# Performance work log

Measured on AMD Instinct MI355X. Metric: run time of the kernel, lower is better.

The kernel has to match this reference:

```python
import jax, jax.numpy as jnp
import numpy as np

FDS = [80, 160, 400, 600]
N, E, G, IN = 20000, 320000, 128, 3072
EPS = 1e-5  # BatchNorm1d default eps


def setup_inputs():
    key = jax.random.key(0)
    ks = iter(jax.random.split(key, 64))
    inp = {}
    inp["x"] = jax.random.normal(next(ks), (N, IN), jnp.float32)
    inp["edge_index"] = jax.random.randint(next(ks), (2, E), 0, N)
    inp["batch"] = jnp.sort(jax.random.randint(next(ks), (N,), 0, G))
    for i, fd in enumerate(FDS):
        din = IN if i == 0 else FDS[i - 1]
        def u(shape, fan):
            s = 1.0 / np.sqrt(fan)
            return jax.random.uniform(next(ks), shape, jnp.float32, -s, s)
        inp[f"wa{i}"] = u((din, 4 * fd), din)      # Linear(din, 4*fd)
        inp[f"ba{i}"] = u((4 * fd,), din)
        inp[f"wb{i}"] = u((4 * fd, fd), 4 * fd)    # Linear(4*fd, fd)
        inp[f"bb{i}"] = u((fd,), 4 * fd)
        inp[f"gw{i}"] = u((fd, fd), fd)            # GCNConv weight
        inp[f"gb{i}"] = jnp.zeros((fd,), jnp.float32)  # GCNConv bias
        inp[f"gamma{i}"] = jnp.ones((fd,), jnp.float32)
        inp[f"beta{i}"] = jnp.zeros((fd,), jnp.float32)
        inp[f"mean{i}"] = jax.random.normal(next(ks), (fd,), jnp.float32) * 0.1
        inp[f"var{i}"] = jax.random.uniform(next(ks), (fd,), jnp.float32, 0.5, 1.5)
    return inp


def _gcn_edges(edge_index, n):
    # GCNConv default: add self-loops, symmetric D^-1/2 (A+I) D^-1/2 normalization
    loops = jnp.arange(n)
    src = jnp.concatenate([edge_index[0], loops])
    dst = jnp.concatenate([edge_index[1], loops])
    deg = jax.ops.segment_sum(jnp.ones(src.shape, jnp.float32), dst, num_segments=n)
    dinv = jnp.where(deg > 0, jax.lax.rsqrt(deg), 0.0)
    return src, dst, dinv[src] * dinv[dst]


def _forward(x, edge_index, batch, params):
    src, dst, norm = _gcn_edges(edge_index, N)
    for (wa, ba, wb, bb, gw, gb, gamma, beta, mean, var) in params:
        h = jax.nn.relu(x @ wa + ba)   # dropout = identity in eval mode
        h = jax.nn.relu(h @ wb + bb)
        h = h @ gw                     # GCN linear transform
        # gather -> normalize -> scatter-add message passing, then bias
        h = jax.ops.segment_sum(h[src] * norm[:, None], dst, num_segments=N) + gb
        # BatchNorm1d (eval: running stats)
        h = (h - mean) * jax.lax.rsqrt(var + EPS) * gamma + beta
        x = jax.nn.relu(h)             # residual branch is dead: dims never match
    return jax.ops.segment_max(x, batch, num_segments=G)  # global_max_pool


def reference(x, edge_index, batch,
              wa0, ba0, wb0, bb0, gw0, gb0, gamma0, beta0, mean0, var0,
              wa1, ba1, wb1, bb1, gw1, gb1, gamma1, beta1, mean1, var1,
              wa2, ba2, wb2, bb2, gw2, gb2, gamma2, beta2, mean2, var2,
              wa3, ba3, wb3, bb3, gw3, gb3, gamma3, beta3, mean3, var3):
    params = [
        (wa0, ba0, wb0, bb0, gw0, gb0, gamma0, beta0, mean0, var0),
        (wa1, ba1, wb1, bb1, gw1, gb1, gamma1, beta1, mean1, var1),
        (wa2, ba2, wb2, bb2, gw2, gb2, gamma2, beta2, mean2, var2),
        (wa3, ba3, wb3, bb3, gw3, gb3, gamma3, beta3, mean3, var3),
    ]
    return _forward(x, edge_index, batch, params)
```

## Files before the change

### kernel.cpp

```cpp
#include <hip/hip_runtime.h>
#include <cstdint>
#include <cstddef>
#include <cmath>


#define EPS_BN 1e-5f

typedef unsigned short u16;
typedef short short8 __attribute__((ext_vector_type(8)));
typedef u16 u16x8 __attribute__((ext_vector_type(8)));
typedef u16 u16x4 __attribute__((ext_vector_type(4)));
typedef float fx4 __attribute__((ext_vector_type(4)));

__device__ __forceinline__ u16 bf16_rn(float f) {
  unsigned u = __float_as_uint(f);
  return (u16)((u + 0x7FFFu + ((u >> 16) & 1u)) >> 16);
}
__device__ __forceinline__ float bf16_f(u16 h) {
  return __uint_as_float(((unsigned)h) << 16);
}

__device__ __forceinline__ void gload16(const void* g, void* l) {
  __builtin_amdgcn_global_load_lds(
      (const __attribute__((address_space(1))) void*)g,
      (__attribute__((address_space(3))) void*)l, 16, 0, 0);
}

__device__ __forceinline__ void map_tile(int b, int tm, int tn, int T,
                                         int& mt, int& nt) {
  const int x = b & 7;
  const int s = b >> 3;
  const int cap = ((tm - x + 7) >> 3) * tn;
  if (s < cap) {
    const int q = s / tn;
    mt = x + (q << 3);
    nt = s - q * tn;
    return;
  }
  int r = s - cap;
  for (int xp = 0; xp < x; ++xp) {
    const int nbp = (T - xp + 7) >> 3;
    const int capp = ((tm - xp + 7) >> 3) * tn;
    if (nbp > capp) r += nbp - capp;
  }
  for (int xq = 0; xq < 8; ++xq) {
    const int nbq = (T - xq + 7) >> 3;
    const int capq = ((tm - xq + 7) >> 3) * tn;
    const int def = capq - nbq;
    if (def > 0) {
      if (r < def) {
        const int sq = nbq + r;
        const int q = sq / tn;
        mt = xq + (q << 3);
        nt = sq - q * tn;
        return;
      }
      r -= def;
    }
  }
  mt = 0; nt = 0;
}

template <int OUTMODE, bool SPLITA>
__global__ __launch_bounds__(256, 2) void gemm_mfma(
    const u16* __restrict__ Ahi, const u16* __restrict__ Alo,
    const float* __restrict__ Af,
    const u16* __restrict__ Bhi, const u16* __restrict__ Blo,
    const float* __restrict__ bias,
    float* __restrict__ Cf, u16* __restrict__ Chi, u16* __restrict__ Clo,
    int M, int N, int K, int lda, int ldb, int ldc, int tm, int tn) {
  __shared__ __align__(16) u16 As[2][128 * 32];
  __shared__ __align__(16) u16 Bs[2][128 * 32];

  int mt, nt;
  map_tile(blockIdx.x, tm, tn, tm * tn, mt, nt);
  const int m0 = mt * 128;
  const int n0 = nt * 128;

  const int tid = threadIdx.x;
  const int lane = tid & 63;
  const int wid = tid >> 6;
  const int wm = (wid >> 1) * 64;
  const int wn = (wid & 1) * 64;
  const int quad = lane >> 4;
  const int l15 = lane & 15;

  const int srow = tid >> 2;
  const int sg = ((tid & 3) ^ srow ^ (srow >> 2)) & 3;
  int ar0 = m0 + srow;      if (ar0 >= M) ar0 = M - 1;
  int ar1 = m0 + srow + 64; if (ar1 >= M) ar1 = M - 1;
  int br0 = n0 + srow;      if (br0 >= N) br0 = N - 1;
  int br1 = n0 + srow + 64; if (br1 >= N) br1 = N - 1;
  const size_t aof0 = (size_t)ar0 * lda + (sg << 3);
  const size_t aof1 = (size_t)ar1 * lda + (sg << 3);
  const size_t bof0 = (size_t)br0 * ldb + (sg << 3);
  const size_t bof1 = (size_t)br1 * ldb + (sg << 3);
  const int l0 = wid << 9;
  const int l1 = 2048 + (wid << 9);
  const int wls = srow * 32 + ((tid & 3) << 3);

  fx4 zf = {0.f, 0.f, 0.f, 0.f};
  fx4 acc[4][4];
#pragma unroll
  for (int a = 0; a < 4; ++a)
#pragma unroll
    for (int b = 0; b < 4; ++b) acc[a][b] = zf;

  const int nk = (K + 31) >> 5;
  for (int ki = 0; ki < nk; ++ki) {
    const int k0 = ki << 5;
    u16x8 va_h[2], va_l[2];
    if (SPLITA) {
#pragma unroll
      for (int it = 0; it < 2; ++it) {
        const float* pp = Af + (it ? aof1 : aof0) + k0;
        const fx4 f0 = *(const fx4*)pp;
        const fx4 f1 = *(const fx4*)(pp + 4);
        u16x8 h, l;
#pragma unroll
        for (int j = 0; j < 4; ++j) {
          const u16 hb = bf16_rn(f0[j]);
          h[j] = hb;
          l[j] = bf16_rn(f0[j] - bf16_f(hb));
        }
#pragma unroll
        for (int j = 0; j < 4; ++j) {
          const u16 hb = bf16_rn(f1[j]);
          h[4 + j] = hb;
          l[4 + j] = bf16_rn(f1[j] - bf16_f(hb));
        }
        va_h[it] = h;
        va_l[it] = l;
      }
    }

    if (ki) __syncthreads();

    if (SPLITA) {
      gload16(Bhi + bof0 + k0, &Bs[0][l0]);
      gload16(Bhi + bof1 + k0, &Bs[0][l1]);
      gload16(Blo + bof0 + k0, &Bs[1][l0]);
      gload16(Blo + bof1 + k0, &Bs[1][l1]);
      *(u16x8*)&As[0][wls] = va_h[0];
      *(u16x8*)&As[0][wls + 2048] = va_h[1];
      *(u16x8*)&As[1][wls] = va_l[0];
      *(u16x8*)&As[1][wls + 2048] = va_l[1];
    } else {
      gload16(Ahi + aof0 + k0, &As[0][l0]);
      gload16(Ahi + aof1 + k0, &As[0][l1]);
      gload16(Alo + aof0 + k0, &As[1][l0]);
      gload16(Alo + aof1 + k0, &As[1][l1]);
      gload16(Bhi + bof0 + k0, &Bs[0][l0]);
      gload16(Bhi + bof1 + k0, &Bs[0][l1]);
      gload16(Blo + bof0 + k0, &Bs[1][l0]);
      gload16(Blo + bof1 + k0, &Bs[1][l1]);
    }
    __syncthreads();

    short8 ah[4], al[4], bh[4], bl[4];
#pragma unroll
    for (int t = 0; t < 4; ++t) {
      const int rA = wm + t * 16 + l15;
      const int oa = rA * 32 + (((quad ^ rA ^ (rA >> 2)) & 3) << 3);
      ah[t] = *(const short8*)&As[0][oa];
      al[t] = *(const short8*)&As[1][oa];
      const int rB = wn + t * 16 + l15;
      const int ob = rB * 32 + (((quad ^ rB ^ (rB >> 2)) & 3) << 3);
      bh[t] = *(const short8*)&Bs[0][ob];
      bl[t] = *(const short8*)&Bs[1][ob];
    }
#pragma unroll
    for (int a = 0; a < 4; ++a)
#pragma unroll
      for (int b = 0; b < 4; ++b) {
        acc[a][b] = __builtin_amdgcn_mfma_f32_16x16x32_bf16(ah[a], bh[b], acc[a][b], 0, 0, 0);
        acc[a][b] = __builtin_amdgcn_mfma_f32_16x16x32_bf16(ah[a], bl[b], acc[a][b], 0, 0, 0);
        acc[a][b] = __builtin_amdgcn_mfma_f32_16x16x32_bf16(al[a], bh[b], acc[a][b], 0, 0, 0);
      }
  }

#pragma unroll
  for (int a = 0; a < 4; ++a)
#pragma unroll
    for (int b = 0; b < 4; ++b) {
      const int gn = n0 + wn + b * 16 + l15;
      if (gn >= ldc) continue;
      const bool live = gn < N;
      const float bv = (OUTMODE == 1 && live) ? bias[gn] : 0.f;
#pragma unroll
      for (int r = 0; r < 4; ++r) {
        const int gm = m0 + wm + a * 16 + quad * 4 + r;
        if (gm >= M) continue;
        float v = live ? acc[a][b][r] : 0.f;
        if (OUTMODE == 1) {
          v = live ? fmaxf(v + bv, 0.f) : 0.f;
          const u16 hb = bf16_rn(v);
          Chi[(size_t)gm * ldc + gn] = hb;
          Clo[(size_t)gm * ldc + gn] = bf16_rn(v - bf16_f(hb));
        } else {
          Cf[(size_t)gm * ldc + gn] = v;
        }
      }
    }
}

struct TSJob { const float* W; u16* Th; u16* Tl; int K; int Kp; int N; int tiles_k; int base; };
struct TSJobs { TSJob j[12]; };

__global__ __launch_bounds__(256) void transpose_split_all(TSJobs jobs, int njobs) {
  const int b = blockIdx.x;
  int ji = 0;
  while (ji + 1 < njobs && jobs.j[ji + 1].base <= b) ++ji;
  const TSJob J = jobs.j[ji];
  const int t = b - J.base;
  const int k0 = (t % J.tiles_k) * 32;
  const int n0 = (t / J.tiles_k) * 32;
  __shared__ float tile[32][33];
  const int tx = threadIdx.x & 31, ty = threadIdx.x >> 5;
#pragma unroll
  for (int i = 0; i < 32; i += 8) {
    const int k = k0 + ty + i, n = n0 + tx;
    tile[ty + i][tx] = (k < J.K && n < J.N) ? J.W[(size_t)k * J.N + n] : 0.f;
  }
  __syncthreads();
#pragma unroll
  for (int i = 0; i < 32; i += 8) {
    const int n = n0 + ty + i, k = k0 + tx;
    if (n < J.N && k < J.Kp) {
      const float f = tile[tx][ty + i];
      const u16 hb = bf16_rn(f);
      J.Th[(size_t)n * J.Kp + k] = hb;
      J.Tl[(size_t)n * J.Kp + k] = bf16_rn(f - bf16_f(hb));
    }
  }
}

__global__ void count_deg(const int* __restrict__ dst, int E, int* __restrict__ cnt) {
  int e = blockIdx.x * blockDim.x + threadIdx.x;
  if (e < E) atomicAdd(&cnt[dst[e]], 1);
}

__global__ void compute_dinv(const int* __restrict__ cnt, float* __restrict__ dinv, int N) {
  int i = blockIdx.x * blockDim.x + threadIdx.x;
  if (i < N) dinv[i] = rsqrtf((float)(cnt[i] + 1));
}

__global__ void scan_block(const int* __restrict__ cnt, int* __restrict__ partial,
                           int* __restrict__ blocksum, int N) {
  __shared__ int s[256];
  const int t = threadIdx.x;
  const int i = blockIdx.x * 256 + t;
  int v = (i < N) ? cnt[i] : 0;
  s[t] = v;
  __syncthreads();
  for (int off = 1; off < 256; off <<= 1) {
    int u = (t >= off) ? s[t - off] : 0;
    __syncthreads();
    s[t] += u;
    __syncthreads();
  }
  if (i < N) partial[i] = s[t];
  if (t == 255) blocksum[blockIdx.x] = s[255];
}

__global__ void scan_sums(int* __restrict__ blocksum, int NB) {
  __shared__ int s[256];
  const int t = threadIdx.x;
  int v = (t < NB) ? blocksum[t] : 0;
  s[t] = v;
  __syncthreads();
  for (int off = 1; off < 256; off <<= 1) {
    int u = (t >= off) ? s[t - off] : 0;
    __syncthreads();
    s[t] += u;
    __syncthreads();
  }
  if (t < NB) blocksum[t] = s[t] - v;
}

__global__ void finalize_rowptr(const int* __restrict__ partial, const int* __restrict__ blockoff,
                                int* __restrict__ rowptr, int N) {
  int i = blockIdx.x * 256 + threadIdx.x;
  if (i < N) rowptr[i + 1] = partial[i] + blockoff[blockIdx.x];
  if (i == 0) rowptr[0] = 0;
}

__global__ void fill_csr(const int* __restrict__ src, const int* __restrict__ dst, int E,
                         const int* __restrict__ rowptr, int* __restrict__ cursor,
                         int* __restrict__ colidx) {
  int e = blockIdx.x * blockDim.x + threadIdx.x;
  if (e < E) {
    int d = dst[e];
    int p = atomicAdd(&cursor[d], 1);
    colidx[rowptr[d] + p] = src[e];
  }
}

__global__ void mp_bn_relu(
    const float* __restrict__ H, const int* __restrict__ rowptr,
    const int* __restrict__ colidx, const float* __restrict__ dinv,
    const float* __restrict__ gb, const float* __restrict__ gamma,
    const float* __restrict__ beta, const float* __restrict__ mean,
    const float* __restrict__ var,
    u16* __restrict__ Xh, u16* __restrict__ Xl, int N, int F, int Fp) {
  const int nch = Fp >> 2;
  const int idx = blockIdx.x * blockDim.x + threadIdx.x;
  if (idx >= N * nch) return;
  const int i = idx / nch;
  const int c = idx - i * nch;
  const size_t rowi = (size_t)i * Fp + (c << 2);
  if ((c << 2) >= F) {
    const u16x4 z = {0, 0, 0, 0};
    *(u16x4*)(Xh + rowi) = z;
    *(u16x4*)(Xl + rowi) = z;
    return;
  }
  const float di = dinv[i];
  fx4 acc = (di * di) * *(const fx4*)(H + rowi);
  const int e0 = rowptr[i], e1 = rowptr[i + 1];
  int e = e0;
  for (; e + 4 <= e1; e += 4) {
    const int s0 = colidx[e + 0], s1 = colidx[e + 1];
    const int s2 = colidx[e + 2], s3 = colidx[e + 3];
    const float w0 = di * dinv[s0], w1 = di * dinv[s1];
    const float w2 = di * dinv[s2], w3 = di * dinv[s3];
    const fx4 v0 = *(const fx4*)(H + (size_t)s0 * Fp + (c << 2));
    const fx4 v1 = *(const fx4*)(H + (size_t)s1 * Fp + (c << 2));
    const fx4 v2 = *(const fx4*)(H + (size_t)s2 * Fp + (c << 2));
    const fx4 v3 = *(const fx4*)(H + (size_t)s3 * Fp + (c << 2));
    acc += w0 * v0;
    acc += w1 * v1;
    acc += w2 * v2;
    acc += w3 * v3;
  }
  for (; e < e1; ++e) {
    const int s = colidx[e];
    acc += (di * dinv[s]) * *(const fx4*)(H + (size_t)s * Fp + (c << 2));
  }
  u16x4 oh, ol;
#pragma unroll
  for (int j = 0; j < 4; ++j) {
    const int col = (c << 2) + j;
    float v = (acc[j] + gb[col] - mean[col]) * rsqrtf(var[col] + EPS_BN) * gamma[col] + beta[col];
    v = fmaxf(v, 0.f);
    const u16 hb = bf16_rn(v);
    oh[j] = hb;
    ol[j] = bf16_rn(v - bf16_f(hb));
  }
  *(u16x4*)(Xh + rowi) = oh;
  *(u16x4*)(Xl + rowi) = ol;
}

__global__ void pool_seg(const u16* __restrict__ Xh, const u16* __restrict__ Xl,
                         const int* __restrict__ batch, float* __restrict__ out,
                         int N, int F, int ldx) {
  const int g = blockIdx.x;
  int lo = 0, hi = N;
  while (lo < hi) { int m = (lo + hi) >> 1; if (batch[m] < g) lo = m + 1; else hi = m; }
  const int s0 = lo;
  hi = N;
  while (lo < hi) { int m = (lo + hi) >> 1; if (batch[m] <= g) lo = m + 1; else hi = m; }
  const int s1 = lo;
  const int c = threadIdx.x;
  if (c * 4 >= F) return;
  fx4 mx = {-INFINITY, -INFINITY, -INFINITY, -INFINITY};
  for (int i = s0; i < s1; ++i) {
    const size_t off = (size_t)i * ldx + (c << 2);
    const u16x4 h = *(const u16x4*)(Xh + off);
    const u16x4 l = *(const u16x4*)(Xl + off);
#pragma unroll
    for (int j = 0; j < 4; ++j) mx[j] = fmaxf(mx[j], bf16_f(h[j]) + bf16_f(l[j]));
  }
  *(fx4*)(out + (size_t)g * F + (c << 2)) = mx;
}

extern "C" void kernel_launch(void* const* d_in, const int* in_sizes, int n_in,
                              void* d_out, int out_size, void* d_ws, size_t ws_size,
                              hipStream_t stream) {
  const float* x = (const float*)d_in[0];
  const int* edges = (const int*)d_in[1];
  const int* batch = (const int*)d_in[2];
  const int E = in_sizes[1] / 2;
  const int Nn = in_sizes[2];

  static const int FDS[4]  = {80, 160, 400, 600};
  static const int FDP[4]  = {96, 160, 416, 608};
  static const int DINS[4] = {3072, 80, 160, 400};
  static const int DINP[4] = {3072, 96, 160, 416};
  const float *wa[4], *ba[4], *wb[4], *bb[4], *gw[4], *gb[4], *gamma[4], *beta[4], *mean[4], *var[4];
  for (int i = 0; i < 4; ++i) {
    const int b = 3 + 10 * i;
    wa[i] = (const float*)d_in[b + 0];
    ba[i] = (const float*)d_in[b + 1];
    wb[i] = (const float*)d_in[b + 2];
    bb[i] = (const float*)d_in[b + 3];
    gw[i] = (const float*)d_in[b + 4];
    gb[i] = (const float*)d_in[b + 5];
    gamma[i] = (const float*)d_in[b + 6];
    beta[i] = (const float*)d_in[b + 7];
    mean[i] = (const float*)d_in[b + 8];
    var[i] = (const float*)d_in[b + 9];
  }

  char* p = (char*)d_ws;
  auto alloc = [&](size_t bytes) {
    char* r = p;
    p += (bytes + 255) & ~(size_t)255;
    return r;
  };
  u16* actA_h = (u16*)alloc((size_t)Nn * 2400 * 2);
  u16* actA_l = (u16*)alloc((size_t)Nn * 2400 * 2);
  u16* actB_h = (u16*)alloc((size_t)Nn * 608 * 2);
  u16* actB_l = (u16*)alloc((size_t)Nn * 608 * 2);
  float* H3 = (float*)actA_h;

  u16 *waT_h[4], *waT_l[4], *wbT_h[4], *wbT_l[4], *gwT_h[4], *gwT_l[4];
  for (int i = 0; i < 4; ++i) {
    const size_t s1 = (size_t)4 * FDS[i] * DINP[i];
    const size_t s2 = (size_t)FDS[i] * 4 * FDS[i];
    const size_t s3 = (size_t)FDS[i] * FDP[i];
    waT_h[i] = (u16*)alloc(s1 * 2);
    waT_l[i] = (u16*)alloc(s1 * 2);
    wbT_h[i] = (u16*)alloc(s2 * 2);
    wbT_l[i] = (u16*)alloc(s2 * 2);
    gwT_h[i] = (u16*)alloc(s3 * 2);
    gwT_l[i] = (u16*)alloc(s3 * 2);
  }

  int* cnt = (int*)alloc((size_t)Nn * sizeof(int));
  int* cursor = (int*)alloc((size_t)Nn * sizeof(int));
  int* partial = (int*)alloc((size_t)Nn * sizeof(int));
  int* blocksum = (int*)alloc(256 * sizeof(int));
  int* rowptr = (int*)alloc((size_t)(Nn + 1) * sizeof(int));
  int* colidx = (int*)alloc((size_t)E * sizeof(int));
  float* dinv = (float*)alloc((size_t)Nn * sizeof(float));

  const int* srcIdx = edges;
  const int* dstIdx = edges + E;

  {
    TSJobs jobs;
    int base = 0, ji = 0;
    auto addjob = [&](const float* W, int K, int Kp, int Ncols, u16* Th, u16* Tl) {
      const int tk = Kp / 32, tn = (Ncols + 31) / 32;
      jobs.j[ji++] = TSJob{W, Th, Tl, K, Kp, Ncols, tk, base};
      base += tk * tn;
    };
    for (int i = 0; i < 4; ++i) {
      addjob(wa[i], DINS[i], DINP[i], 4 * FDS[i], waT_h[i], waT_l[i]);
      addjob(wb[i], 4 * FDS[i], 4 * FDS[i], FDS[i], wbT_h[i], wbT_l[i]);
      addjob(gw[i], FDS[i], FDP[i], FDS[i], gwT_h[i], gwT_l[i]);
    }
    transpose_split_all<<<base, 256, 0, stream>>>(jobs, 12);
  }

  hipMemsetAsync(cnt, 0, (size_t)Nn * sizeof(int), stream);
  hipMemsetAsync(cursor, 0, (size_t)Nn * sizeof(int), stream);

  const int EB = (E + 255) / 256;
  const int NB = (Nn + 255) / 256;
  count_deg<<<EB, 256, 0, stream>>>(dstIdx, E, cnt);
  compute_dinv<<<NB, 256, 0, stream>>>(cnt, dinv, Nn);
  scan_block<<<NB, 256, 0, stream>>>(cnt, partial, blocksum, Nn);
  scan_sums<<<1, 256, 0, stream>>>(blocksum, NB);
  finalize_rowptr<<<NB, 256, 0, stream>>>(partial, blocksum, rowptr, Nn);
  fill_csr<<<EB, 256, 0, stream>>>(srcIdx, dstIdx, E, rowptr, cursor, colidx);

  const int tm = (Nn + 127) / 128;
  for (int i = 0; i < 4; ++i) {
    const int fd = FDS[i], fdp = FDP[i];
    const int hid = 4 * fd;
    const int din = DINS[i], dinp = DINP[i];

    {
      const int tn = (hid + 127) / 128;
      if (i == 0) {
        gemm_mfma<1, true><<<tm * tn, 256, 0, stream>>>(
            nullptr, nullptr, x, waT_h[0], waT_l[0], ba[0],
            nullptr, actA_h, actA_l, Nn, hid, din, din, dinp, hid, tm, tn);
      } else {
        gemm_mfma<1, false><<<tm * tn, 256, 0, stream>>>(
            actB_h, actB_l, nullptr, waT_h[i], waT_l[i], ba[i],
            nullptr, actA_h, actA_l, Nn, hid, din, dinp, dinp, hid, tm, tn);
      }
    }
    {
      const int tn = (fd + 127) / 128;
      gemm_mfma<1, false><<<tm * tn, 256, 0, stream>>>(
          actA_h, actA_l, nullptr, wbT_h[i], wbT_l[i], bb[i],
          nullptr, actB_h, actB_l, Nn, fd, hid, hid, hid, fdp, tm, tn);
    }
    {
      const int tn = (fd + 127) / 128;
      gemm_mfma<0, false><<<tm * tn, 256, 0, stream>>>(
          actB_h, actB_l, nullptr, gwT_h[i], gwT_l[i], nullptr,
          H3, nullptr, nullptr, Nn, fd, fd, fdp, fdp, fdp, tm, tn);
    }
    {
      const int items = Nn * (fdp >> 2);
      mp_bn_relu<<<(items + 255) / 256, 256, 0, stream>>>(
          H3, rowptr, colidx, dinv, gb[i], gamma[i], beta[i], mean[i], var[i],
          actB_h, actB_l, Nn, fd, fdp);
    }
  }

  pool_seg<<<out_size / 600, 192, 0, stream>>>(actB_h, actB_l, batch, (float*)d_out,
                                               Nn, 600, 608);
}
```

Before: 1.692 ms.

## Add double-buffered, phase-interleaved MFMA GEMM for bf16-split activation inputs

Splits the GEMM into a dedicated fp32-input split kernel and a new double-buffered kernel for pre-split bf16 inputs. The new kernel prefetches tiles two steps ahead into a second LDS buffer and waits with explicit vmcnt. Within each K step it issues the next tile's global-to-LDS loads spread across waves, interleaved between MFMA sub-blocks. It also raises MFMA priority with s_setprio, aiming to hide load latency behind compute. LDS use doubles to 64KB per block, which may hurt occupancy at 2 blocks per CU, and the many barriers add sync overhead.

Result: slower. 1.850 ms (+9.3%).

```diff
diff --git a/kernel.cpp b/kernel.cpp
--- a/kernel.cpp
+++ b/kernel.cpp
@@ -25,6 +25,8 @@
       (const __attribute__((address_space(1))) void*)g,
       (__attribute__((address_space(3))) void*)l, 16, 0, 0);
 }
+
+#define MEMFENCE() asm volatile("" ::: "memory")
 
 __device__ __forceinline__ void map_tile(int b, int tm, int tn, int T,
                                          int& mt, int& nt) {
@@ -61,13 +63,165 @@
   mt = 0; nt = 0;
 }
 
-template <int OUTMODE, bool SPLITA>
-__global__ __launch_bounds__(256, 2) void gemm_mfma(
+template <int OUTMODE>
+__global__ __launch_bounds__(256, 2) void gemm_ph(
     const u16* __restrict__ Ahi, const u16* __restrict__ Alo,
+    const u16* __restrict__ Bhi, const u16* __restrict__ Blo,
+    const float* __restrict__ bias,
+    float* __restrict__ Cf, u16* __restrict__ Chi, u16* __restrict__ Clo,
+    int M, int N, int K, int lda, int ldb, int ldc, int tm, int tn) {
+  __shared__ __align__(16) u16 As[2][2][128 * 32];
+  __shared__ __align__(16) u16 Bs[2][2][128 * 32];
+
+  int mt, nt;
+  map_tile(blockIdx.x, tm, tn, tm * tn, mt, nt);
+  const int m0 = mt * 128;
+  const int n0 = nt * 128;
+
+  const int tid = threadIdx.x;
+  const int lane = tid & 63;
+  const int wid = tid >> 6;
+  const int wm = (wid >> 1) * 64;
+  const int wn = (wid & 1) * 64;
+  const int quad = lane >> 4;
+  const int l15 = lane & 15;
+
+  const int srow = tid >> 2;
+  const int sg = ((tid & 3) ^ srow ^ (srow >> 2)) & 3;
+  int ar0 = m0 + srow;      if (ar0 >= M) ar0 = M - 1;
+  int ar1 = m0 + srow + 64; if (ar1 >= M) ar1 = M - 1;
+  int br0 = n0 + srow;      if (br0 >= N) br0 = N - 1;
+  int br1 = n0 + srow + 64; if (br1 >= N) br1 = N - 1;
+  const size_t aof0 = (size_t)ar0 * lda + (sg << 3);
+  const size_t aof1 = (size_t)ar1 * lda + (sg << 3);
+  const size_t bof0 = (size_t)br0 * ldb + (sg << 3);
+  const size_t bof1 = (size_t)br1 * ldb + (sg << 3);
+  const int l0 = wid << 9;
+  const int l1 = 2048 + (wid << 9);
+
+  fx4 zf = {0.f, 0.f, 0.f, 0.f};
+  fx4 acc[4][4];
+#pragma unroll
+  for (int a = 0; a < 4; ++a)
+#pragma unroll
+    for (int b = 0; b < 4; ++b) acc[a][b] = zf;
+
+  const int nk = (K + 31) >> 5;
+
+  auto stageA = [&](int kt, int bufi) {
+    const size_t kk = (size_t)kt << 5;
+    gload16(Ahi + aof0 + kk, &As[bufi][0][l0]);
+    gload16(Ahi + aof1 + kk, &As[bufi][0][l1]);
+    gload16(Alo + aof0 + kk, &As[bufi][1][l0]);
+    gload16(Alo + aof1 + kk, &As[bufi][1][l1]);
+  };
+  auto stageB = [&](int kt, int bufi) {
+    const size_t kk = (size_t)kt << 5;
+    gload16(Bhi + bof0 + kk, &Bs[bufi][0][l0]);
+    gload16(Bhi + bof1 + kk, &Bs[bufi][0][l1]);
+    gload16(Blo + bof0 + kk, &Bs[bufi][1][l0]);
+    gload16(Blo + bof1 + kk, &Bs[bufi][1][l1]);
+  };
+
+  stageA(0, 0); stageB(0, 0);
+  if (nk > 1) { stageA(1, 1); stageB(1, 1); }
+  if (nk > 1) asm volatile("s_waitcnt vmcnt(8)" ::: "memory");
+  else        asm volatile("s_waitcnt vmcnt(0)" ::: "memory");
+  __builtin_amdgcn_s_barrier();
+  MEMFENCE();
+
+  for (int ki = 0; ki < nk; ++ki) {
+    const int cur = ki & 1;
+    const bool st = (ki + 2) < nk;
+
+    short8 bh[4], bl[4], ah, al;
+#pragma unroll
+    for (int t = 0; t < 4; ++t) {
+      const int rB = wn + t * 16 + l15;
+      const int ob = rB * 32 + (((quad ^ rB ^ (rB >> 2)) & 3) << 3);
+      bh[t] = *(const short8*)&Bs[cur][0][ob];
+      bl[t] = *(const short8*)&Bs[cur][1][ob];
+    }
+    {
+      const int rA = wm + l15;
+      const int oa = rA * 32 + (((quad ^ rA ^ (rA >> 2)) & 3) << 3);
+      ah = *(const short8*)&As[cur][0][oa];
+      al = *(const short8*)&As[cur][1][oa];
+    }
+    __builtin_amdgcn_s_setprio(1);
+#pragma unroll
+    for (int b = 0; b < 4; ++b) {
+      acc[0][b] = __builtin_amdgcn_mfma_f32_16x16x32_bf16(ah, bh[b], acc[0][b], 0, 0, 0);
+      acc[0][b] = __builtin_amdgcn_mfma_f32_16x16x32_bf16(ah, bl[b], acc[0][b], 0, 0, 0);
+      acc[0][b] = __builtin_amdgcn_mfma_f32_16x16x32_bf16(al, bh[b], acc[0][b], 0, 0, 0);
+    }
+    __builtin_amdgcn_s_setprio(0);
+    MEMFENCE();
+    __builtin_amdgcn_s_barrier();
+    MEMFENCE();
+
+#pragma unroll
+    for (int t = 1; t < 4; ++t) {
+      const int rA = wm + t * 16 + l15;
+      const int oa = rA * 32 + (((quad ^ rA ^ (rA >> 2)) & 3) << 3);
+      ah = *(const short8*)&As[cur][0][oa];
+      al = *(const short8*)&As[cur][1][oa];
+      if (t == 1 && st) {
+        stageB(ki + 2, cur);
+        if (wid == 0) stageA(ki + 2, cur);
+      }
+      if (t == 2 && st && wid == 1) stageA(ki + 2, cur);
+      if (t == 3 && st && wid == 2) stageA(ki + 2, cur);
+      __builtin_amdgcn_s_setprio(1);
+#pragma unroll
+      for (int b = 0; b < 4; ++b) {
+        acc[t][b] = __builtin_amdgcn_mfma_f32_16x16x32_bf16(ah, bh[b], acc[t][b], 0, 0, 0);
+        acc[t][b] = __builtin_amdgcn_mfma_f32_16x16x32_bf16(ah, bl[b], acc[t][b], 0, 0, 0);
+        acc[t][b] = __builtin_amdgcn_mfma_f32_16x16x32_bf16(al, bh[b], acc[t][b], 0, 0, 0);
+      }
+      __builtin_amdgcn_s_setprio(0);
+      MEMFENCE();
+      __builtin_amdgcn_s_barrier();
+      MEMFENCE();
+    }
+    if (st && wid == 3) stageA(ki + 2, cur);
+    if (st)                asm volatile("s_waitcnt vmcnt(8)" ::: "memory");
+    else if (ki + 1 < nk)  asm volatile("s_waitcnt vmcnt(0)" ::: "memory");
+    MEMFENCE();
+    __builtin_amdgcn_s_barrier();
+    MEMFENCE();
+  }
+
+#pragma unroll
+  for (int a = 0; a < 4; ++a)
+#pragma unroll
+    for (int b = 0; b < 4; ++b) {
+      const int gn = n0 + wn + b * 16 + l15;
+      if (gn >= ldc) continue;
+      const bool live = gn < N;
+      const float bv = (OUTMODE == 1 && live) ? bias[gn] : 0.f;
+#pragma unroll
+      for (int r = 0; r < 4; ++r) {
+        const int gm = m0 + wm + a * 16 + quad * 4 + r;
+        if (gm >= M) continue;
+        float v = live ? acc[a][b][r] : 0.f;
+        if (OUTMODE == 1) {
+          v = live ? fmaxf(v + bv, 0.f) : 0.f;
+          const u16 hb = bf16_rn(v);
+          Chi[(size_t)gm * ldc + gn] = hb;
+          Clo[(size_t)gm * ldc + gn] = bf16_rn(v - bf16_f(hb));
+        } else {
+          Cf[(size_t)gm * ldc + gn] = v;
+        }
+      }
+    }
+}
+
+__global__ __launch_bounds__(256, 2) void gemm_splita(
     const float* __restrict__ Af,
     const u16* __restrict__ Bhi, const u16* __restrict__ Blo,
     const float* __restrict__ bias,
-    float* __restrict__ Cf, u16* __restrict__ Chi, u16* __restrict__ Clo,
+    u16* __restrict__ Chi, u16* __restrict__ Clo,
     int M, int N, int K, int lda, int ldb, int ldc, int tm, int tn) {
   __shared__ __align__(16) u16 As[2][128 * 32];
   __shared__ __align__(16) u16 Bs[2][128 * 32];
@@ -110,51 +264,38 @@
   for (int ki = 0; ki < nk; ++ki) {
     const int k0 = ki << 5;
     u16x8 va_h[2], va_l[2];
-    if (SPLITA) {
-#pragma unroll
-      for (int it = 0; it < 2; ++it) {
-        const float* pp = Af + (it ? aof1 : aof0) + k0;
-        const fx4 f0 = *(const fx4*)pp;
-        const fx4 f1 = *(const fx4*)(pp + 4);
-        u16x8 h, l;
-#pragma unroll
-        for (int j = 0; j < 4; ++j) {
-          const u16 hb = bf16_rn(f0[j]);
-          h[j] = hb;
-          l[j] = bf16_rn(f0[j] - bf16_f(hb));
-        }
-#pragma unroll
-        for (int j = 0; j < 4; ++j) {
-          const u16 hb = bf16_rn(f1[j]);
-          h[4 + j] = hb;
-          l[4 + j] = bf16_rn(f1[j] - bf16_f(hb));
-        }
-        va_h[it] = h;
-        va_l[it] = l;
-      }
+#pragma unroll
+    for (int it = 0; it < 2; ++it) {
+      const float* pp = Af + (it ? aof1 : aof0) + k0;
+      const fx4 f0 = *(const fx4*)pp;
+      const fx4 f1 = *(const fx4*)(pp + 4);
+      u16x8 h, l;
+#pragma unroll
+      for (int j = 0; j < 4; ++j) {
+        const u16 hb = bf16_rn(f0[j]);
+        h[j] = hb;
+        l[j] = bf16_rn(f0[j] - bf16_f(hb));
+      }
+#pragma unroll
+      for (int j = 0; j < 4; ++j) {
+        const u16 hb = bf16_rn(f1[j]);
+        h[4 + j] = hb;
+        l[4 + j] = bf16_rn(f1[j] - bf16_f(hb));
+      }
+      va_h[it] = h;
+      va_l[it] = l;
     }
 
     if (ki) __syncthreads();
 
-    if (SPLITA) {
-      gload16(Bhi + bof0 + k0, &Bs[0][l0]);
-      gload16(Bhi + bof1 + k0, &Bs[0][l1]);
-      gload16(Blo + bof0 + k0, &Bs[1][l0]);
-      gload16(Blo + bof1 + k0, &Bs[1][l1]);
-      *(u16x8*)&As[0][wls] = va_h[0];
-      *(u16x8*)&As[0][wls + 2048] = va_h[1];
-      *(u16x8*)&As[1][wls] = va_l[0];
-      *(u16x8*)&As[1][wls + 2048] = va_l[1];
-    } else {
-      gload16(Ahi + aof0 + k0, &As[0][l0]);
-      gload16(Ahi + aof1 + k0, &As[0][l1]);
-      gload16(Alo + aof0 + k0, &As[1][l0]);
-      gload16(Alo + aof1 + k0, &As[1][l1]);
-      gload16(Bhi + bof0 + k0, &Bs[0][l0]);
-      gload16(Bhi + bof1 + k0, &Bs[0][l1]);
-      gload16(Blo + bof0 + k0, &Bs[1][l0]);
-      gload16(Blo + bof1 + k0, &Bs[1][l1]);
-    }
+    gload16(Bhi + bof0 + k0, &Bs[0][l0]);
+    gload16(Bhi + bof1 + k0, &Bs[0][l1]);
+    gload16(Blo + bof0 + k0, &Bs[1][l0]);
+    gload16(Blo + bof1 + k0, &Bs[1][l1]);
+    *(u16x8*)&As[0][wls] = va_h[0];
+    *(u16x8*)&As[0][wls + 2048] = va_h[1];
+    *(u16x8*)&As[1][wls] = va_l[0];
+    *(u16x8*)&As[1][wls + 2048] = va_l[1];
     __syncthreads();
 
     short8 ah[4], al[4], bh[4], bl[4];
@@ -186,19 +327,15 @@
       const int gn = n0 + wn + b * 16 + l15;
       if (gn >= ldc) continue;
       const bool live = gn < N;
-      const float bv = (OUTMODE == 1 && live) ? bias[gn] : 0.f;
+      const float bv = live ? bias[gn] : 0.f;
 #pragma unroll
       for (int r = 0; r < 4; ++r) {
         const int gm = m0 + wm + a * 16 + quad * 4 + r;
-        if (gm >= M) continue;
-        float v = live ? acc[a][b][r] : 0.f;
-        if (OUTMODE == 1) {
-          v = live ? fmaxf(v + bv, 0.f) : 0.f;
+        if (gm < M) {
+          float v = live ? fmaxf(acc[a][b][r] + bv, 0.f) : 0.f;
           const u16 hb = bf16_rn(v);
           Chi[(size_t)gm * ldc + gn] = hb;
           Clo[(size_t)gm * ldc + gn] = bf16_rn(v - bf16_f(hb));
-        } else {
-          Cf[(size_t)gm * ldc + gn] = v;
         }
       }
     }
@@ -475,25 +612,25 @@
     {
       const int tn = (hid + 127) / 128;
       if (i == 0) {
-        gemm_mfma<1, true><<<tm * tn, 256, 0, stream>>>(
-            nullptr, nullptr, x, waT_h[0], waT_l[0], ba[0],
-            nullptr, actA_h, actA_l, Nn, hid, din, din, dinp, hid, tm, tn);
+        gemm_splita<<<tm * tn, 256, 0, stream>>>(
+            x, waT_h[0], waT_l[0], ba[0],
+            actA_h, actA_l, Nn, hid, din, din, dinp, hid, tm, tn);
       } else {
-        gemm_mfma<1, false><<<tm * tn, 256, 0, stream>>>(
-            actB_h, actB_l, nullptr, waT_h[i], waT_l[i], ba[i],
+        gemm_ph<1><<<tm * tn, 256, 0, stream>>>(
+            actB_h, actB_l, waT_h[i], waT_l[i], ba[i],
             nullptr, actA_h, actA_l, Nn, hid, din, dinp, dinp, hid, tm, tn);
       }
     }
     {
       const int tn = (fd + 127) / 128;
-      gemm_mfma<1, false><<<tm * tn, 256, 0, stream>>>(
-          actA_h, actA_l, nullptr, wbT_h[i], wbT_l[i], bb[i],
+      gemm_ph<1><<<tm * tn, 256, 0, stream>>>(
+          actA_h, actA_l, wbT_h[i], wbT_l[i], bb[i],
           nullptr, actB_h, actB_l, Nn, fd, hid, hid, hid, fdp, tm, tn);
     }
     {
       const int tn = (fd + 127) / 128;
-      gemm_mfma<0, false><<<tm * tn, 256, 0, stream>>>(
-          actB_h, actB_l, nullptr, gwT_h[i], gwT_l[i], nullptr,
+      gemm_ph<0><<<tm * tn, 256, 0, stream>>>(
+          actB_h, actB_l, gwT_h[i], gwT_l[i], nullptr,
           H3, nullptr, nullptr, Nn, fd, fd, fdp, fdp, fdp, tm, tn);
     }
     {
```
